# Kernel tuning notes

Measured on AMD Instinct MI355X. Metric: run time of the kernel, lower is better.

## Reference

```python
import jax, jax.numpy as jnp
import numpy as np

EPS = 1e-08
TEMPERATURE = 1.0
HEADS = 4
OUT_DIM = 32
IN_DIM = 128
N_NODES = 100000
N_EDGES = 1600000


def setup_inputs() -> dict:
    key = jax.random.key(0)
    k1, k2, k3, k4, k5, k6 = jax.random.split(key, 6)
    x = jax.random.normal(k1, (N_NODES, IN_DIM), dtype=jnp.float32)
    # nn.Linear(in_dim, heads*out_dim, bias=False).weight -> [heads*out_dim, in_dim]
    W = jax.random.normal(k2, (HEADS * OUT_DIM, IN_DIM), dtype=jnp.float32) * 0.05
    a_src = jax.random.normal(k3, (HEADS, OUT_DIM), dtype=jnp.float32) * 0.1
    a_dst = jax.random.normal(k4, (HEADS, OUT_DIM), dtype=jnp.float32) * 0.1
    edge_index = jax.random.randint(k5, (2, N_EDGES), 0, N_NODES, dtype=jnp.int32)
    rnbrw_weights = jax.random.uniform(k6, (N_EDGES,), dtype=jnp.float32)
    return {"x": x, "W": W, "a_src": a_src, "a_dst": a_dst,
            "edge_index": edge_index, "rnbrw_weights": rnbrw_weights}


def reference(x, W, a_src, a_dst, edge_index, rnbrw_weights):
    N = x.shape[0]
    heads, out_dim = a_src.shape
    # h = W(x).view(N, heads, out_dim)
    h = (x @ W.T).reshape(N, heads, out_dim)
    src, dst = edge_index[0], edge_index[1]
    h_src = h[src]  # [E, heads, out_dim]
    h_dst = h[dst]  # [E, heads, out_dim]
    # per-edge attention scores [E, heads]
    score = jnp.einsum('ehd,hd->eh', h_src, a_src) + jnp.einsum('ehd,hd->eh', h_dst, a_dst)
    # strategy == 'pre_softmax_bias'
    score = score + jnp.log(rnbrw_weights + EPS)[:, None]
    score = jnp.where(score >= 0, score, 0.2 * score)  # leaky_relu(0.2)
    scaled = score / TEMPERATURE
    # edge softmax over incoming edges of each dst node
    seg_max = jax.ops.segment_max(scaled, dst, num_segments=N)      # [N, heads]
    exp_s = jnp.exp(scaled - seg_max[dst])                           # [E, heads]
    denom = jax.ops.segment_sum(exp_s, dst, num_segments=N)         # [N, heads]
    alpha = exp_s / (denom[dst] + EPS)                               # [E, heads]
    # scatter-add aggregation: out[dst] += alpha * h_src
    out = jax.ops.segment_sum(alpha[..., None] * h_src, dst, num_segments=N)
    out = out.reshape(N, heads * out_dim)
    return out, alpha
```

## Files before the change

kernel.cpp:

```cpp
#include <hip/hip_runtime.h>

#define EPS 1e-8f

__device__ inline unsigned short f2bf(float f) {
    unsigned u = __float_as_uint(f);
    unsigned r = u + 0x7fffu + ((u >> 16) & 1u);
    return (unsigned short)(r >> 16);
}
__device__ inline float bflo(unsigned v) { return __uint_as_float(v << 16); }
__device__ inline float bfhi(unsigned v) { return __uint_as_float(v & 0xffff0000u); }

__global__ __launch_bounds__(256) void gemm_s_kernel(
    const float* __restrict__ x, const float* __restrict__ W,
    const float* __restrict__ a_src, const float* __restrict__ a_dst,
    unsigned short* __restrict__ hb, float* __restrict__ s_src, float* __restrict__ s_dst,
    int N, int n_tiles)
{
    __shared__ float Wt[128 * 64];
    __shared__ float xt[128 * 64];

    const int t = threadIdx.x;
    const int half = blockIdx.y;
    const float* Wh = W + half * 64 * 128;

#pragma unroll
    for (int p = 0; p < 8; ++p) {
        int idx = p * 256 + t;
        int ol = (idx & 31) | ((idx >> 10) << 5);
        int k4 = (idx >> 5) & 31;
        float4 w = *(const float4*)(Wh + ol * 128 + k4 * 4);
        Wt[(4 * k4 + 0) * 64 + ol] = w.x;
        Wt[(4 * k4 + 1) * 64 + ol] = w.y;
        Wt[(4 * k4 + 2) * 64 + ol] = w.z;
        Wt[(4 * k4 + 3) * 64 + ol] = w.w;
    }
    __syncthreads();

    const int o4 = t & 15;
    const int n4g = t >> 4;
    const int head = half * 2 + (o4 >> 3);
    const float4 as = *(const float4*)(a_src + head * 32 + (o4 & 7) * 4);
    const float4 ad = *(const float4*)(a_dst + head * 32 + (o4 & 7) * 4);

    for (int tile = blockIdx.x; tile < n_tiles; tile += gridDim.x) {
        const int nbase = tile * 64;
        __syncthreads();
#pragma unroll
        for (int p = 0; p < 8; ++p) {
            int idx = p * 256 + t;
            int n = idx & 63;
            int k4 = idx >> 6;
            int ng = nbase + n;
            float4 v = make_float4(0.f, 0.f, 0.f, 0.f);
            if (ng < N) v = *(const float4*)(x + (size_t)ng * 128 + k4 * 4);
            xt[(4 * k4 + 0) * 64 + n] = v.x;
            xt[(4 * k4 + 1) * 64 + n] = v.y;
            xt[(4 * k4 + 2) * 64 + n] = v.z;
            xt[(4 * k4 + 3) * 64 + n] = v.w;
        }
        __syncthreads();

        float acc[4][4];
#pragma unroll
        for (int i = 0; i < 4; ++i)
#pragma unroll
            for (int j = 0; j < 4; ++j) acc[i][j] = 0.f;

        for (int k = 0; k < 128; ++k) {
            float4 wv = *(const float4*)(Wt + k * 64 + 4 * o4);
            float4 xv = *(const float4*)(xt + k * 64 + 4 * n4g);
            float wa[4] = {wv.x, wv.y, wv.z, wv.w};
            float xa[4] = {xv.x, xv.y, xv.z, xv.w};
#pragma unroll
            for (int i = 0; i < 4; ++i)
#pragma unroll
                for (int j = 0; j < 4; ++j) acc[i][j] += xa[i] * wa[j];
        }

#pragma unroll
        for (int i = 0; i < 4; ++i) {
            int n = nbase + 4 * n4g + i;
            float ps = acc[i][0] * as.x + acc[i][1] * as.y + acc[i][2] * as.z + acc[i][3] * as.w;
            float pd = acc[i][0] * ad.x + acc[i][1] * ad.y + acc[i][2] * ad.z + acc[i][3] * ad.w;
            ps += __shfl_xor(ps, 1); ps += __shfl_xor(ps, 2); ps += __shfl_xor(ps, 4);
            pd += __shfl_xor(pd, 1); pd += __shfl_xor(pd, 2); pd += __shfl_xor(pd, 4);
            if (n < N) {
                ushort4 hv;
                hv.x = f2bf(acc[i][0]); hv.y = f2bf(acc[i][1]);
                hv.z = f2bf(acc[i][2]); hv.w = f2bf(acc[i][3]);
                *(ushort4*)(hb + (size_t)n * 128 + half * 64 + 4 * o4) = hv;
                if ((o4 & 7) == 0) {
                    s_src[n * 4 + head] = ps;
                    s_dst[n * 4 + head] = pd;
                }
            }
        }
    }
}

__global__ __launch_bounds__(256) void edge_score_kernel(
    const int* __restrict__ src, const int* __restrict__ dst,
    const float* __restrict__ rnbrw,
    const float* __restrict__ s_src, const float* __restrict__ s_dst,
    float* __restrict__ es_orig, int* __restrict__ counts, int E)
{
    int e = blockIdx.x * 256 + threadIdx.x;
    if (e >= E) return;
    int s = src[e], d = dst[e];
    float lw = __logf(rnbrw[e] + EPS);
    float4 a = *(const float4*)(s_src + s * 4);
    float4 b = *(const float4*)(s_dst + d * 4);
    float sc[4] = {a.x + b.x + lw, a.y + b.y + lw, a.z + b.z + lw, a.w + b.w + lw};
    float es[4];
#pragma unroll
    for (int hh = 0; hh < 4; ++hh) {
        float v = sc[hh];
        v = (v >= 0.f) ? v : 0.2f * v;
        es[hh] = __expf(v);
    }
    *(float4*)(es_orig + (size_t)e * 4) = make_float4(es[0], es[1], es[2], es[3]);
    atomicAdd(counts + d, 1);
}

__global__ __launch_bounds__(256) void scan1_kernel(
    const int* __restrict__ counts, int* __restrict__ offs, int* __restrict__ bsum, int N)
{
    __shared__ int sh[256];
    int t = threadIdx.x;
    int base = blockIdx.x * 1024 + t * 4;
    int c[4];
#pragma unroll
    for (int j = 0; j < 4; ++j) c[j] = (base + j < N) ? counts[base + j] : 0;
    int tsum = c[0] + c[1] + c[2] + c[3];
    sh[t] = tsum;
    __syncthreads();
    for (int off = 1; off < 256; off <<= 1) {
        int v = (t >= off) ? sh[t - off] : 0;
        __syncthreads();
        sh[t] += v;
        __syncthreads();
    }
    int run = sh[t] - tsum;
    if (t == 255) bsum[blockIdx.x] = sh[255];
#pragma unroll
    for (int j = 0; j < 4; ++j) {
        if (base + j < N) { offs[base + j] = run; run += c[j]; }
    }
}

__global__ void scan2_kernel(int* __restrict__ bsum, int nb)
{
    if (threadIdx.x == 0) {
        int acc = 0;
        for (int i = 0; i < nb; ++i) { int v = bsum[i]; bsum[i] = acc; acc += v; }
    }
}

__global__ __launch_bounds__(256) void scan3_kernel(
    int* __restrict__ offs, const int* __restrict__ bsum,
    int* __restrict__ cursor, int N)
{
    int i = blockIdx.x * 256 + threadIdx.x;
    if (i >= N) return;
    int v = offs[i] + bsum[i >> 10];
    offs[i] = v;
    cursor[i] = v;
}

__global__ __launch_bounds__(256) void scatter_kernel(
    const int* __restrict__ src, const int* __restrict__ dst,
    int* __restrict__ cursor, int2* __restrict__ rec,
    int E, int ssz, int bps)
{
    const int shard = blockIdx.x & 7;
    const int j = blockIdx.x >> 3;
    const int lo = shard * ssz;
    const int hi = lo + ssz;
    const int stride = bps * 256;
    for (int base = j * 256; base < E; base += stride) {
        int e = base + threadIdx.x;
        if (e < E) {
            int d = dst[e];
            if (d >= lo && d < hi) {
                int pos = atomicAdd(cursor + d, 1);
                rec[pos] = make_int2(src[e], e);
            }
        }
    }
}

__global__ __launch_bounds__(256) void node_aggr_kernel(
    const int* __restrict__ offs, const int* __restrict__ counts,
    const int2* __restrict__ rec, const float* __restrict__ es_orig,
    const unsigned short* __restrict__ hb,
    float* __restrict__ inv_den, float* __restrict__ out, int N)
{
    int gid = blockIdx.x * 256 + threadIdx.x;
    int n = gid >> 5;
    int l = gid & 31;
    if (n >= N) return;

    const int q    = l & 15;
    const int half = l >> 4;
    const int head = q >> 2;

    const int beg = offs[n];
    const int cnt = counts[n];

    float a0 = 0.f, a1 = 0.f, a2 = 0.f, a3 = 0.f;
    float a4 = 0.f, a5 = 0.f, a6 = 0.f, a7 = 0.f;
    float den = 0.f;

    for (int i = 0; i < cnt; i += 4) {
        int j0 = i + half;
        int j1 = i + 2 + half;
        int jc0 = (j0 < cnt) ? j0 : 0;
        int jc1 = (j1 < cnt) ? j1 : 0;
        int2 r0 = rec[(size_t)beg + jc0];
        int2 r1 = rec[(size_t)beg + jc1];
        uint4 v0 = *(const uint4*)(hb + (size_t)r0.x * 128 + q * 8);
        uint4 v1 = *(const uint4*)(hb + (size_t)r1.x * 128 + q * 8);
        float e0 = es_orig[(size_t)r0.y * 4 + head];
        float e1 = es_orig[(size_t)r1.y * 4 + head];
        if (j0 >= cnt) e0 = 0.f;
        if (j1 >= cnt) e1 = 0.f;
        a0 += e0 * bflo(v0.x); a1 += e0 * bfhi(v0.x);
        a2 += e0 * bflo(v0.y); a3 += e0 * bfhi(v0.y);
        a4 += e0 * bflo(v0.z); a5 += e0 * bfhi(v0.z);
        a6 += e0 * bflo(v0.w); a7 += e0 * bfhi(v0.w);
        a0 += e1 * bflo(v1.x); a1 += e1 * bfhi(v1.x);
        a2 += e1 * bflo(v1.y); a3 += e1 * bfhi(v1.y);
        a4 += e1 * bflo(v1.z); a5 += e1 * bfhi(v1.z);
        a6 += e1 * bflo(v1.w); a7 += e1 * bfhi(v1.w);
        den += e0 + e1;
    }

    a0 += __shfl_xor(a0, 16, 32); a1 += __shfl_xor(a1, 16, 32);
    a2 += __shfl_xor(a2, 16, 32); a3 += __shfl_xor(a3, 16, 32);
    a4 += __shfl_xor(a4, 16, 32); a5 += __shfl_xor(a5, 16, 32);
    a6 += __shfl_xor(a6, 16, 32); a7 += __shfl_xor(a7, 16, 32);
    den += __shfl_xor(den, 16, 32);

    const float inv = 1.f / (den + EPS);

    float d0 = __shfl(den, 0, 32);
    float d1 = __shfl(den, 4, 32);
    float d2 = __shfl(den, 8, 32);
    float d3 = __shfl(den, 12, 32);

    float4 o = half ? make_float4(a4 * inv, a5 * inv, a6 * inv, a7 * inv)
                    : make_float4(a0 * inv, a1 * inv, a2 * inv, a3 * inv);
    *(float4*)(out + (size_t)n * 128 + q * 8 + half * 4) = o;

    if (l == 0)
        *(float4*)(inv_den + (size_t)n * 4) =
            make_float4(1.f / (d0 + EPS), 1.f / (d1 + EPS),
                        1.f / (d2 + EPS), 1.f / (d3 + EPS));
}

__global__ __launch_bounds__(256) void alpha_kernel(
    const int* __restrict__ dst, const float* __restrict__ inv_den,
    float* __restrict__ alpha, int E)
{
    int e = blockIdx.x * 256 + threadIdx.x;
    if (e >= E) return;
    int d = dst[e];
    float4 es = *(const float4*)(alpha + (size_t)e * 4);
    float4 iv = *(const float4*)(inv_den + (size_t)d * 4);
    es.x *= iv.x; es.y *= iv.y; es.z *= iv.z; es.w *= iv.w;
    *(float4*)(alpha + (size_t)e * 4) = es;
}

extern "C" void kernel_launch(void* const* d_in, const int* in_sizes, int n_in,
                              void* d_out, int out_size, void* d_ws, size_t ws_size,
                              hipStream_t stream) {
    const float* x      = (const float*)d_in[0];
    const float* W      = (const float*)d_in[1];
    const float* a_src  = (const float*)d_in[2];
    const float* a_dst  = (const float*)d_in[3];
    const int*   eidx   = (const int*)d_in[4];
    const float* rnbrw  = (const float*)d_in[5];

    const int E = in_sizes[5];
    const int N = in_sizes[0] / 128;

    float* out   = (float*)d_out;
    float* alpha = out + (size_t)N * 128;
    float* es_orig = alpha;

    char* w = (char*)d_ws;
    unsigned short* hb = (unsigned short*)w;  w += (size_t)N * 128 * 2;
    int* counts  = (int*)w;                   w += (size_t)N * 4;
    int* offs    = (int*)w;                   w += (size_t)N * 4;
    int* cursor  = (int*)w;                   w += (size_t)N * 4;
    int* bsum    = (int*)w;                   w += 512;
    float* inv_den = (float*)w;               w += (size_t)N * 4 * 4;
    int2* rec    = (int2*)w;
    float* s_src = (float*)w;
    float* s_dst = s_src + (size_t)N * 4;

    const int* src = eidx;
    const int* dst = eidx + E;

    hipMemsetAsync(counts, 0, (size_t)N * sizeof(int), stream);

    int n_tiles = (N + 63) / 64;
    dim3 gridA(512, 2);
    gemm_s_kernel<<<gridA, 256, 0, stream>>>(x, W, a_src, a_dst, hb, s_src, s_dst, N, n_tiles);

    int eblocks = (E + 255) / 256;
    edge_score_kernel<<<eblocks, 256, 0, stream>>>(src, dst, rnbrw, s_src, s_dst,
                                                   es_orig, counts, E);

    int nb = (N + 1023) / 1024;
    scan1_kernel<<<nb, 256, 0, stream>>>(counts, offs, bsum, N);
    scan2_kernel<<<1, 64, 0, stream>>>(bsum, nb);
    scan3_kernel<<<(N + 255) / 256, 256, 0, stream>>>(offs, bsum, cursor, N);

    int ssz = (N + 7) / 8;
    int bps = 256;
    scatter_kernel<<<8 * bps, 256, 0, stream>>>(src, dst, cursor, rec, E, ssz, bps);

    int ablocks = ((size_t)N * 32 + 255) / 256;
    node_aggr_kernel<<<ablocks, 256, 0, stream>>>(offs, counts, rec, es_orig, hb,
                                                  inv_den, out, N);

    alpha_kernel<<<eblocks, 256, 0, stream>>>(dst, inv_den, alpha, E);
}
```

Baseline: 436.4 us.

## Compute edge scores during CSR scatter and recompute them in alpha pass

The separate edge-score pass is removed. Counting becomes its own small atomic kernel. Scores are computed inside the CSR scatter kernel and written in destination-sorted order, so node aggregation reads them contiguously instead of gathering by original edge id. The alpha kernel recomputes scores from s_src/s_dst instead of reading stored exps. This trades one full edge pass and random gathers for recomputed exp/log work and a larger workspace (E*20 bytes).

```diff
diff --git a/kernel.cpp b/kernel.cpp
--- a/kernel.cpp
+++ b/kernel.cpp
@@ -98,28 +98,11 @@
     }
 }
 
-__global__ __launch_bounds__(256) void edge_score_kernel(
-    const int* __restrict__ src, const int* __restrict__ dst,
-    const float* __restrict__ rnbrw,
-    const float* __restrict__ s_src, const float* __restrict__ s_dst,
-    float* __restrict__ es_orig, int* __restrict__ counts, int E)
+__global__ __launch_bounds__(256) void count_kernel(
+    const int* __restrict__ dst, int* __restrict__ counts, int E)
 {
     int e = blockIdx.x * 256 + threadIdx.x;
-    if (e >= E) return;
-    int s = src[e], d = dst[e];
-    float lw = __logf(rnbrw[e] + EPS);
-    float4 a = *(const float4*)(s_src + s * 4);
-    float4 b = *(const float4*)(s_dst + d * 4);
-    float sc[4] = {a.x + b.x + lw, a.y + b.y + lw, a.z + b.z + lw, a.w + b.w + lw};
-    float es[4];
-#pragma unroll
-    for (int hh = 0; hh < 4; ++hh) {
-        float v = sc[hh];
-        v = (v >= 0.f) ? v : 0.2f * v;
-        es[hh] = __expf(v);
-    }
-    *(float4*)(es_orig + (size_t)e * 4) = make_float4(es[0], es[1], es[2], es[3]);
-    atomicAdd(counts + d, 1);
+    if (e < E) atomicAdd(counts + dst[e], 1);
 }
 
 __global__ __launch_bounds__(256) void scan1_kernel(
@@ -167,9 +150,11 @@
     cursor[i] = v;
 }
 
-__global__ __launch_bounds__(256) void scatter_kernel(
+__global__ __launch_bounds__(256) void scatter_score_kernel(
     const int* __restrict__ src, const int* __restrict__ dst,
-    int* __restrict__ cursor, int2* __restrict__ rec,
+    const float* __restrict__ rnbrw,
+    const float* __restrict__ s_src, const float* __restrict__ s_dst,
+    int* __restrict__ cursor, float* __restrict__ csr_es, int* __restrict__ csr_src,
     int E, int ssz, int bps)
 {
     const int shard = blockIdx.x & 7;
@@ -179,19 +164,28 @@
     const int stride = bps * 256;
     for (int base = j * 256; base < E; base += stride) {
         int e = base + threadIdx.x;
-        if (e < E) {
-            int d = dst[e];
-            if (d >= lo && d < hi) {
-                int pos = atomicAdd(cursor + d, 1);
-                rec[pos] = make_int2(src[e], e);
-            }
-        }
+        if (e >= E) continue;
+        int d = dst[e];
+        if (d < lo || d >= hi) continue;
+        int s = src[e];
+        float lw = __logf(rnbrw[e] + EPS);
+        float4 a = *(const float4*)(s_src + s * 4);
+        float4 b = *(const float4*)(s_dst + d * 4);
+        float4 es;
+        float v;
+        v = a.x + b.x + lw; v = (v >= 0.f) ? v : 0.2f * v; es.x = __expf(v);
+        v = a.y + b.y + lw; v = (v >= 0.f) ? v : 0.2f * v; es.y = __expf(v);
+        v = a.z + b.z + lw; v = (v >= 0.f) ? v : 0.2f * v; es.z = __expf(v);
+        v = a.w + b.w + lw; v = (v >= 0.f) ? v : 0.2f * v; es.w = __expf(v);
+        int pos = atomicAdd(cursor + d, 1);
+        *(float4*)(csr_es + (size_t)pos * 4) = es;
+        csr_src[pos] = s;
     }
 }
 
 __global__ __launch_bounds__(256) void node_aggr_kernel(
     const int* __restrict__ offs, const int* __restrict__ counts,
-    const int2* __restrict__ rec, const float* __restrict__ es_orig,
+    const int* __restrict__ csr_src, const float* __restrict__ csr_es,
     const unsigned short* __restrict__ hb,
     float* __restrict__ inv_den, float* __restrict__ out, int N)
 {
@@ -216,12 +210,12 @@
         int j1 = i + 2 + half;
         int jc0 = (j0 < cnt) ? j0 : 0;
         int jc1 = (j1 < cnt) ? j1 : 0;
-        int2 r0 = rec[(size_t)beg + jc0];
-        int2 r1 = rec[(size_t)beg + jc1];
-        uint4 v0 = *(const uint4*)(hb + (size_t)r0.x * 128 + q * 8);
-        uint4 v1 = *(const uint4*)(hb + (size_t)r1.x * 128 + q * 8);
-        float e0 = es_orig[(size_t)r0.y * 4 + head];
-        float e1 = es_orig[(size_t)r1.y * 4 + head];
+        int s0 = csr_src[(size_t)beg + jc0];
+        int s1 = csr_src[(size_t)beg + jc1];
+        uint4 v0 = *(const uint4*)(hb + (size_t)s0 * 128 + q * 8);
+        uint4 v1 = *(const uint4*)(hb + (size_t)s1 * 128 + q * 8);
+        float e0 = csr_es[(size_t)(beg + jc0) * 4 + head];
+        float e1 = csr_es[(size_t)(beg + jc1) * 4 + head];
         if (j0 >= cnt) e0 = 0.f;
         if (j1 >= cnt) e1 = 0.f;
         a0 += e0 * bflo(v0.x); a1 += e0 * bfhi(v0.x);
@@ -259,16 +253,25 @@
 }
 
 __global__ __launch_bounds__(256) void alpha_kernel(
-    const int* __restrict__ dst, const float* __restrict__ inv_den,
-    float* __restrict__ alpha, int E)
+    const int* __restrict__ src, const int* __restrict__ dst,
+    const float* __restrict__ rnbrw,
+    const float* __restrict__ s_src, const float* __restrict__ s_dst,
+    const float* __restrict__ inv_den, float* __restrict__ alpha, int E)
 {
     int e = blockIdx.x * 256 + threadIdx.x;
     if (e >= E) return;
-    int d = dst[e];
-    float4 es = *(const float4*)(alpha + (size_t)e * 4);
+    int s = src[e], d = dst[e];
+    float lw = __logf(rnbrw[e] + EPS);
+    float4 a = *(const float4*)(s_src + s * 4);
+    float4 b = *(const float4*)(s_dst + d * 4);
     float4 iv = *(const float4*)(inv_den + (size_t)d * 4);
-    es.x *= iv.x; es.y *= iv.y; es.z *= iv.z; es.w *= iv.w;
-    *(float4*)(alpha + (size_t)e * 4) = es;
+    float4 al;
+    float v;
+    v = a.x + b.x + lw; v = (v >= 0.f) ? v : 0.2f * v; al.x = __expf(v) * iv.x;
+    v = a.y + b.y + lw; v = (v >= 0.f) ? v : 0.2f * v; al.y = __expf(v) * iv.y;
+    v = a.z + b.z + lw; v = (v >= 0.f) ? v : 0.2f * v; al.z = __expf(v) * iv.z;
+    v = a.w + b.w + lw; v = (v >= 0.f) ? v : 0.2f * v; al.w = __expf(v) * iv.w;
+    *(float4*)(alpha + (size_t)e * 4) = al;
 }
 
 extern "C" void kernel_launch(void* const* d_in, const int* in_sizes, int n_in,
@@ -286,31 +289,30 @@
 
     float* out   = (float*)d_out;
     float* alpha = out + (size_t)N * 128;
-    float* es_orig = alpha;
 
     char* w = (char*)d_ws;
     unsigned short* hb = (unsigned short*)w;  w += (size_t)N * 128 * 2;
+    float* csr_es = (float*)w;                w += (size_t)E * 16;
+    int* csr_src  = (int*)w;                  w += (size_t)E * 4;
+    float* s_src  = (float*)w;                w += (size_t)N * 16;
+    float* s_dst  = (float*)w;                w += (size_t)N * 16;
+    float* inv_den = (float*)w;               w += (size_t)N * 16;
     int* counts  = (int*)w;                   w += (size_t)N * 4;
     int* offs    = (int*)w;                   w += (size_t)N * 4;
     int* cursor  = (int*)w;                   w += (size_t)N * 4;
     int* bsum    = (int*)w;                   w += 512;
-    float* inv_den = (float*)w;               w += (size_t)N * 4 * 4;
-    int2* rec    = (int2*)w;
-    float* s_src = (float*)w;
-    float* s_dst = s_src + (size_t)N * 4;
 
     const int* src = eidx;
     const int* dst = eidx + E;
 
     hipMemsetAsync(counts, 0, (size_t)N * sizeof(int), stream);
+
+    int eblocks = (E + 255) / 256;
+    count_kernel<<<eblocks, 256, 0, stream>>>(dst, counts, E);
 
     int n_tiles = (N + 63) / 64;
     dim3 gridA(512, 2);
     gemm_s_kernel<<<gridA, 256, 0, stream>>>(x, W, a_src, a_dst, hb, s_src, s_dst, N, n_tiles);
-
-    int eblocks = (E + 255) / 256;
-    edge_score_kernel<<<eblocks, 256, 0, stream>>>(src, dst, rnbrw, s_src, s_dst,
-                                                   es_orig, counts, E);
 
     int nb = (N + 1023) / 1024;
     scan1_kernel<<<nb, 256, 0, stream>>>(counts, offs, bsum, N);
@@ -319,11 +321,13 @@
 
     int ssz = (N + 7) / 8;
     int bps = 256;
-    scatter_kernel<<<8 * bps, 256, 0, stream>>>(src, dst, cursor, rec, E, ssz, bps);
+    scatter_score_kernel<<<8 * bps, 256, 0, stream>>>(src, dst, rnbrw, s_src, s_dst,
+                                                      cursor, csr_es, csr_src, E, ssz, bps);
 
     int ablocks = ((size_t)N * 32 + 255) / 256;
-    node_aggr_kernel<<<ablocks, 256, 0, stream>>>(offs, counts, rec, es_orig, hb,
+    node_aggr_kernel<<<ablocks, 256, 0, stream>>>(offs, counts, csr_src, csr_es, hb,
                                                   inv_den, out, N);
 
-    alpha_kernel<<<eblocks, 256, 0, stream>>>(dst, inv_den, alpha, E);
-}
+    alpha_kernel<<<eblocks, 256, 0, stream>>>(src, dst, rnbrw, s_src, s_dst,
+                                              inv_den, alpha, E);
+}
```

Measured after the change: 478.0 us. 1.1x slower.
